# Optimization experiments

Hardware: AMD Instinct MI355X
Metric: run time of the kernel (lower is better)

Reference implementation:

```python
import jax, jax.numpy as jnp
import numpy as np

P, Q, R, H1, H2, PH, B = 32, 32, 8, 128, 64, 16, 8192
PAIRS = P * Q
OUT = PAIRS * R  # X_Z_layer output units


def _pairwise_mask(p, q, r):
    # rows i*q+k correspond to pair (x_i, z_k): connected to x_i and z_k only
    mx = np.zeros((p * q, p), np.float32)
    for i in range(p):
        mx[i * q:(i + 1) * q, i] = 1.0
    mz = np.tile(np.eye(q, dtype=np.float32), (p, 1))
    m = np.concatenate([mx, mz], axis=1)          # [p*q, p+q]
    return np.repeat(m, r, axis=0)                 # [p*q*r, p+q]


def setup_inputs() -> dict:
    key = jax.random.key(0)
    ks = jax.random.split(key, 24)
    rn = lambda k, s, sc=0.1: jax.random.normal(k, s, jnp.float32) * sc
    x = jax.random.normal(ks[0], (B, P), jnp.float32)
    z = jax.random.normal(ks[1], (B, Q), jnp.float32)
    # X_mlp: P -> H1 -> H2 -> 1
    xw1, xb1 = rn(ks[2], (P, H1)), rn(ks[3], (H1,))
    xw2, xb2 = rn(ks[4], (H1, H2)), rn(ks[5], (H2,))
    xw3, xb3 = rn(ks[6], (H2, 1)), rn(ks[7], (1,))
    # Z_mlp: Q -> H1 -> H2 -> 1
    zw1, zb1 = rn(ks[8], (Q, H1)), rn(ks[9], (H1,))
    zw2, zb2 = rn(ks[10], (Q if False else H1, H2)), rn(ks[11], (H2,))
    zw3, zb3 = rn(ks[12], (H2, 1)), rn(ks[13], (1,))
    # masked X_Z_layer: weight pre-multiplied by structured mask (as in __init__)
    mask = jnp.asarray(_pairwise_mask(P, Q, R))    # [OUT, P+Q]
    xzw = (rn(ks[14], (OUT, P + Q)) * mask).T      # [P+Q, OUT]
    xzb = rn(ks[15], (OUT,))
    # 1024 tiny per-pair MLPs: R -> PH (bias) -> 1 (no bias), stacked
    pw1 = rn(ks[16], (PAIRS, R, PH))
    pb1 = rn(ks[17], (PAIRS, PH))
    pw2 = rn(ks[18], (PAIRS, PH))
    return dict(x=x, z=z, xw1=xw1, xb1=xb1, xw2=xw2, xb2=xb2, xw3=xw3, xb3=xb3,
                zw1=zw1, zb1=zb1, zw2=zw2, zb2=zb2, zw3=zw3, zb3=zb3,
                xzw=xzw, xzb=xzb, pw1=pw1, pb1=pb1, pw2=pw2)


def reference(x, z, xw1, xb1, xw2, xb2, xw3, xb3,
              zw1, zb1, zw2, zb2, zw3, zb3, xzw, xzb, pw1, pb1, pw2):
    relu = jax.nn.relu
    # main-effect MLPs
    hx = relu(relu(x @ xw1 + xb1) @ xw2 + xb2)
    out_x = hx @ xw3 + xb3                         # [B,1]
    hz = relu(relu(z @ zw1 + zb1) @ zw2 + zb2)
    out_z = hz @ zw3 + zb3                         # [B,1]
    # masked interaction layer
    xz = jnp.concatenate([x, z], axis=1)           # [B, P+Q]
    h = relu(xz @ xzw + xzb)                       # [B, OUT]
    # all 1024 per-pair MLPs as one batched GEMM
    hp = h.reshape(h.shape[0], PAIRS, R)           # [B, pairs, R]
    t = relu(jnp.einsum('bpr,prh->bph', hp, pw1) + pb1)
    out_xz = jnp.einsum('bph,ph->b', t, pw2)[:, None]  # sum over pairs -> [B,1]
    return out_x + out_z + out_xz
```

## Files before the change

### kernel.cpp

```cpp
#include <hip/hip_runtime.h>

#define B_TOT 8192
#define PP 32
#define QQ 32
#define RR 8
#define H1 128
#define H2 64
#define PHH 16
#define PAIRS 1024
#define OUT_UNITS 8192

typedef float f32x16 __attribute__((ext_vector_type(16)));
typedef short s16x8  __attribute__((ext_vector_type(8)));

union FragU { s16x8 v; unsigned int u[4]; };

__device__ inline unsigned int pack_bf16(float lo, float hi) {
    return __builtin_amdgcn_perm(__float_as_uint(hi), __float_as_uint(lo), 0x07060302u);
}

__global__ void zero_out_k(float* __restrict__ out, int n) {
    int i = blockIdx.x * blockDim.x + threadIdx.x;
    if (i < n) out[i] = 0.f;
}

__global__ __launch_bounds__(256) void main_mlps_k(
    const float* __restrict__ x, const float* __restrict__ z,
    const float* __restrict__ xw1, const float* __restrict__ xb1,
    const float* __restrict__ xw2, const float* __restrict__ xb2,
    const float* __restrict__ xw3, const float* __restrict__ xb3,
    const float* __restrict__ zw1, const float* __restrict__ zb1,
    const float* __restrict__ zw2, const float* __restrict__ zb2,
    const float* __restrict__ zw3, const float* __restrict__ zb3,
    float* __restrict__ out)
{
    const int btile = blockIdx.x;
    const int hf    = blockIdx.y;
    const int which = blockIdx.z;
    const float* in = which ? z   : x;
    const float* w1 = which ? zw1 : xw1;
    const float* b1 = which ? zb1 : xb1;
    const float* w2 = which ? zw2 : xw2;
    const float* b2 = which ? zb2 : xb2;
    const float* w3 = which ? zw3 : xw3;
    const float* b3 = which ? zb3 : xb3;

    __shared__ float inT[32][65];
    __shared__ float h1T[128][65];

    const int t    = threadIdx.x;
    const int w    = __builtin_amdgcn_readfirstlane(t >> 6);
    const int lane = t & 63;
    const int b0   = btile * 64;

    const float4* src = reinterpret_cast<const float4*>(in + (size_t)b0 * 32);
    #pragma unroll
    for (int it = 0; it < 2; ++it) {
        int fi = t + it * 256;
        float4 v = src[fi];
        int bb = fi >> 3;
        int m  = (fi & 7) * 4;
        inT[m][bb] = v.x; inT[m+1][bb] = v.y; inT[m+2][bb] = v.z; inT[m+3][bb] = v.w;
    }
    __syncthreads();

    float h1[32];
    #pragma unroll
    for (int j = 0; j < 32; ++j) h1[j] = b1[w*32 + j];
    #pragma unroll 4
    for (int m = 0; m < 32; ++m) {
        float xv = inT[m][lane];
        #pragma unroll
        for (int j = 0; j < 32; ++j)
            h1[j] = fmaf(xv, w1[m*H1 + w*32 + j], h1[j]);
    }
    #pragma unroll
    for (int j = 0; j < 32; ++j)
        h1T[w*32 + j][lane] = fmaxf(h1[j], 0.f);
    __syncthreads();

    const int n0 = __builtin_amdgcn_readfirstlane(hf*32 + w*8);
    float h2[8];
    #pragma unroll
    for (int n = 0; n < 8; ++n) h2[n] = b2[n0 + n];
    #pragma unroll 4
    for (int m = 0; m < 128; ++m) {
        float hv = h1T[m][lane];
        #pragma unroll
        for (int n = 0; n < 8; ++n)
            h2[n] = fmaf(hv, w2[m*H2 + n0 + n], h2[n]);
    }
    float p = 0.f;
    #pragma unroll
    for (int n = 0; n < 8; ++n)
        p = fmaf(fmaxf(h2[n], 0.f), w3[n0 + n], p);
    if (hf == 0 && w == 0) p += b3[0];
    atomicAdd(out + b0 + lane, p);
}

__global__ __launch_bounds__(256, 3) void interact_k(
    const float* __restrict__ x, const float* __restrict__ z,
    const float* __restrict__ xzw, const float* __restrict__ xzb,
    const float* __restrict__ pw1, const float* __restrict__ pb1,
    const float* __restrict__ pw2, float* __restrict__ out)
{
    __shared__ float zT[16][128];
    __shared__ float4 lwx[16][2];
    __shared__ float4 lwz[16][2];
    __shared__ float4 lhb[16][2];
    __shared__ unsigned lpw1[16][4][16];
    __shared__ float lpb[16][16];
    __shared__ float lpw2[16][16];
    __shared__ float red[128][33];

    const int t     = threadIdx.x;
    const int w     = t >> 6;
    const int lane  = t & 63;
    const int m     = lane & 31;
    const int kh    = lane >> 5;
    const int jj    = m & 15;
    const int cph   = m >> 4;
    const int b0    = blockIdx.x * 128;
    const int y     = blockIdx.y;
    const int i_x   = y >> 1;
    const int k0    = (y & 1) * 16;
    const int pair0 = y * 16;

    {
        int row = t >> 1;
        int c8  = (t & 1) * 8;
        const float* src = z + (size_t)(b0 + row) * 32 + k0 + c8;
        float4 a4 = *reinterpret_cast<const float4*>(src);
        float4 b4 = *reinterpret_cast<const float4*>(src + 4);
        zT[c8+0][row] = a4.x; zT[c8+1][row] = a4.y; zT[c8+2][row] = a4.z; zT[c8+3][row] = a4.w;
        zT[c8+4][row] = b4.x; zT[c8+5][row] = b4.y; zT[c8+6][row] = b4.z; zT[c8+7][row] = b4.w;
    }
    if (t < 128) {
        int p = t >> 3, c = t & 7;
        int gp = pair0 + p;
        reinterpret_cast<float*>(lwx)[t] = xzw[(size_t)i_x * OUT_UNITS + gp*8 + c];
        reinterpret_cast<float*>(lwz)[t] = xzw[(size_t)(32 + k0 + p) * OUT_UNITS + gp*8 + c];
        reinterpret_cast<float*>(lhb)[t] = xzb[gp*8 + c];
    }
    {
        int p = t >> 4, j = t & 15;
        int gp = pair0 + p;
        lpb[p][j]  = pb1[gp*PHH + j];
        lpw2[p][j] = pw2[gp*PHH + j];
    }
    #pragma unroll
    for (int it = 0; it < 4; ++it) {
        int idx = t + it * 256;
        int p = idx >> 6, u = (idx >> 4) & 3, j = idx & 15;
        int gp = pair0 + p;
        float lo = pw1[(size_t)gp * 128 + (2*u)*16 + j];
        float hi = pw1[(size_t)gp * 128 + (2*u+1)*16 + j];
        lpw1[p][u][j] = pack_bf16(lo, hi);
    }

    const int bl  = (w & 1) * 64 + m;
    const float xv0 = x[(size_t)(b0 + bl)      * 32 + i_x];
    const float xv1 = x[(size_t)(b0 + bl + 32) * 32 + i_x];
    __syncthreads();

    f32x16 acc0, acc1, zeroC;
    #pragma unroll
    for (int r = 0; r < 16; ++r) { acc0[r] = 0.f; acc1[r] = 0.f; zeroC[r] = 0.f; }

    const bool realB = (kh == cph);
    const int  ppl0  = (w >> 1) * 4;

    #pragma unroll 2
    for (int kk = 0; kk < 4; ++kk) {
        const int ppl = ppl0 + kk;
        const int pAl = 2*ppl + kh;
        const int pBl = 2*ppl + cph;

        const float zv0 = zT[pAl][bl];
        const float zv1 = zT[pAl][bl + 32];
        const float4 wxa = lwx[pAl][0], wxb = lwx[pAl][1];
        const float4 wza = lwz[pAl][0], wzb = lwz[pAl][1];
        const float4 hba = lhb[pAl][0], hbb = lhb[pAl][1];

        float h0[8], h1[8];
        h0[0] = fmaxf(fmaf(xv0, wxa.x, fmaf(zv0, wza.x, hba.x)), 0.f);
        h0[1] = fmaxf(fmaf(xv0, wxa.y, fmaf(zv0, wza.y, hba.y)), 0.f);
        h0[2] = fmaxf(fmaf(xv0, wxa.z, fmaf(zv0, wza.z, hba.z)), 0.f);
        h0[3] = fmaxf(fmaf(xv0, wxa.w, fmaf(zv0, wza.w, hba.w)), 0.f);
        h0[4] = fmaxf(fmaf(xv0, wxb.x, fmaf(zv0, wzb.x, hbb.x)), 0.f);
        h0[5] = fmaxf(fmaf(xv0, wxb.y, fmaf(zv0, wzb.y, hbb.y)), 0.f);
        h0[6] = fmaxf(fmaf(xv0, wxb.z, fmaf(zv0, wzb.z, hbb.z)), 0.f);
        h0[7] = fmaxf(fmaf(xv0, wxb.w, fmaf(zv0, wzb.w, hbb.w)), 0.f);
        h1[0] = fmaxf(fmaf(xv1, wxa.x, fmaf(zv1, wza.x, hba.x)), 0.f);
        h1[1] = fmaxf(fmaf(xv1, wxa.y, fmaf(zv1, wza.y, hba.y)), 0.f);
        h1[2] = fmaxf(fmaf(xv1, wxa.z, fmaf(zv1, wza.z, hba.z)), 0.f);
        h1[3] = fmaxf(fmaf(xv1, wxa.w, fmaf(zv1, wza.w, hba.w)), 0.f);
        h1[4] = fmaxf(fmaf(xv1, wxb.x, fmaf(zv1, wzb.x, hbb.x)), 0.f);
        h1[5] = fmaxf(fmaf(xv1, wxb.y, fmaf(zv1, wzb.y, hbb.y)), 0.f);
        h1[6] = fmaxf(fmaf(xv1, wxb.z, fmaf(zv1, wzb.z, hbb.z)), 0.f);
        h1[7] = fmaxf(fmaf(xv1, wxb.w, fmaf(zv1, wzb.w, hbb.w)), 0.f);

        FragU a0, a1, bf;
        a0.u[0] = pack_bf16(h0[0], h0[1]);
        a0.u[1] = pack_bf16(h0[2], h0[3]);
        a0.u[2] = pack_bf16(h0[4], h0[5]);
        a0.u[3] = pack_bf16(h0[6], h0[7]);
        a1.u[0] = pack_bf16(h1[0], h1[1]);
        a1.u[1] = pack_bf16(h1[2], h1[3]);
        a1.u[2] = pack_bf16(h1[4], h1[5]);
        a1.u[3] = pack_bf16(h1[6], h1[7]);
        bf.u[0] = realB ? lpw1[pBl][0][jj] : 0u;
        bf.u[1] = realB ? lpw1[pBl][1][jj] : 0u;
        bf.u[2] = realB ? lpw1[pBl][2][jj] : 0u;
        bf.u[3] = realB ? lpw1[pBl][3][jj] : 0u;

        const float pbv = lpb[pBl][jj];
        const float w2v = lpw2[pBl][jj];

        f32x16 d0 = __builtin_amdgcn_mfma_f32_32x32x16_bf16(a0.v, bf.v, zeroC, 0, 0, 0);
        f32x16 d1 = __builtin_amdgcn_mfma_f32_32x32x16_bf16(a1.v, bf.v, zeroC, 0, 0, 0);

        #pragma unroll
        for (int r = 0; r < 16; ++r)
            acc0[r] = fmaf(fmaxf(d0[r] + pbv, 0.f), w2v, acc0[r]);
        #pragma unroll
        for (int r = 0; r < 16; ++r)
            acc1[r] = fmaf(fmaxf(d1[r] + pbv, 0.f), w2v, acc1[r]);
    }

    const int rb0 = (w & 1) * 64;
    if (w < 2) {
        #pragma unroll
        for (int r = 0; r < 16; ++r) {
            int rowf = (r & 3) + 8 * (r >> 2) + 4 * kh;
            red[rb0 + rowf][m]      = acc0[r];
            red[rb0 + 32 + rowf][m] = acc1[r];
        }
    }
    __syncthreads();
    if (w >= 2) {
        #pragma unroll
        for (int r = 0; r < 16; ++r) {
            int rowf = (r & 3) + 8 * (r >> 2) + 4 * kh;
            red[rb0 + rowf][m]      += acc0[r];
            red[rb0 + 32 + rowf][m] += acc1[r];
        }
    }
    __syncthreads();
    if (t < 128) {
        float s = 0.f;
        #pragma unroll
        for (int c = 0; c < 32; ++c) s += red[t][c];
        atomicAdd(out + b0 + t, s);
    }
}

extern "C" void kernel_launch(void* const* d_in, const int* in_sizes, int n_in,
                              void* d_out, int out_size, void* d_ws, size_t ws_size,
                              hipStream_t stream) {
    const float* x   = (const float*)d_in[0];
    const float* z   = (const float*)d_in[1];
    const float* xw1 = (const float*)d_in[2];
    const float* xb1 = (const float*)d_in[3];
    const float* xw2 = (const float*)d_in[4];
    const float* xb2 = (const float*)d_in[5];
    const float* xw3 = (const float*)d_in[6];
    const float* xb3 = (const float*)d_in[7];
    const float* zw1 = (const float*)d_in[8];
    const float* zb1 = (const float*)d_in[9];
    const float* zw2 = (const float*)d_in[10];
    const float* zb2 = (const float*)d_in[11];
    const float* zw3 = (const float*)d_in[12];
    const float* zb3 = (const float*)d_in[13];
    const float* xzw = (const float*)d_in[14];
    const float* xzb = (const float*)d_in[15];
    const float* pw1 = (const float*)d_in[16];
    const float* pb1 = (const float*)d_in[17];
    const float* pw2 = (const float*)d_in[18];
    float* out = (float*)d_out;

    zero_out_k<<<(out_size + 255) / 256, 256, 0, stream>>>(out, out_size);

    main_mlps_k<<<dim3(B_TOT / 64, 2, 2), 256, 0, stream>>>(
        x, z, xw1, xb1, xw2, xb2, xw3, xb3,
        zw1, zb1, zw2, zb2, zw3, zb3, out);

    interact_k<<<dim3(B_TOT / 128, 64), 256, 0, stream>>>(
        x, z, xzw, xzb, pw1, pb1, pw2, out);
}
```

Measured before the change: 141.0 us.

## Fuse main MLPs and interaction kernels into one launch with shared union

Merges the main-effect MLP kernel and the interaction kernel into a single launch that dispatches on block index, with shared memory overlaid through a union. The pair bias is folded into the MFMA accumulator input, main-MLP inputs are read directly into registers instead of being transposed through LDS, and the four per-wave partial sums are reduced in LDS so each block issues one atomic per row. The zeroing kernel becomes a memset. This removes a launch and the tail between the two kernels, cuts atomic traffic, and lets the small MLP blocks overlap the interaction blocks. In exchange, the occupancy hint rises from 3 to 4 blocks per CU, which may pressure registers, and the fused kernel's register use is set by the heavier branch.

```diff
diff --git a/kernel.cpp b/kernel.cpp
--- a/kernel.cpp
+++ b/kernel.cpp
@@ -10,6 +10,9 @@
 #define PAIRS 1024
 #define OUT_UNITS 8192
 
+#define NBLK_IA 4096
+#define NBLK_MM 512
+
 typedef float f32x16 __attribute__((ext_vector_type(16)));
 typedef short s16x8  __attribute__((ext_vector_type(8)));
 
@@ -19,12 +22,24 @@
     return __builtin_amdgcn_perm(__float_as_uint(hi), __float_as_uint(lo), 0x07060302u);
 }
 
-__global__ void zero_out_k(float* __restrict__ out, int n) {
-    int i = blockIdx.x * blockDim.x + threadIdx.x;
-    if (i < n) out[i] = 0.f;
-}
-
-__global__ __launch_bounds__(256) void main_mlps_k(
+union SharedU {
+    struct {
+        float zT[16][128];
+        float4 lwx[16][2];
+        float4 lwz[16][2];
+        float4 lhb[16][2];
+        unsigned lpw1[16][4][16];
+        float lpb[16][16];
+        float lpw2[16][16];
+        float red[128][33];
+    } ia;
+    struct {
+        float h1T[128][65];
+        float red2[4][64];
+    } mm;
+};
+
+__global__ __launch_bounds__(256, 4) void fused_k(
     const float* __restrict__ x, const float* __restrict__ z,
     const float* __restrict__ xw1, const float* __restrict__ xb1,
     const float* __restrict__ xw2, const float* __restrict__ xb2,
@@ -32,226 +47,224 @@
     const float* __restrict__ zw1, const float* __restrict__ zb1,
     const float* __restrict__ zw2, const float* __restrict__ zb2,
     const float* __restrict__ zw3, const float* __restrict__ zb3,
-    float* __restrict__ out)
-{
-    const int btile = blockIdx.x;
-    const int hf    = blockIdx.y;
-    const int which = blockIdx.z;
-    const float* in = which ? z   : x;
-    const float* w1 = which ? zw1 : xw1;
-    const float* b1 = which ? zb1 : xb1;
-    const float* w2 = which ? zw2 : xw2;
-    const float* b2 = which ? zb2 : xb2;
-    const float* w3 = which ? zw3 : xw3;
-    const float* b3 = which ? zb3 : xb3;
-
-    __shared__ float inT[32][65];
-    __shared__ float h1T[128][65];
-
-    const int t    = threadIdx.x;
-    const int w    = __builtin_amdgcn_readfirstlane(t >> 6);
-    const int lane = t & 63;
-    const int b0   = btile * 64;
-
-    const float4* src = reinterpret_cast<const float4*>(in + (size_t)b0 * 32);
-    #pragma unroll
-    for (int it = 0; it < 2; ++it) {
-        int fi = t + it * 256;
-        float4 v = src[fi];
-        int bb = fi >> 3;
-        int m  = (fi & 7) * 4;
-        inT[m][bb] = v.x; inT[m+1][bb] = v.y; inT[m+2][bb] = v.z; inT[m+3][bb] = v.w;
-    }
-    __syncthreads();
-
-    float h1[32];
-    #pragma unroll
-    for (int j = 0; j < 32; ++j) h1[j] = b1[w*32 + j];
-    #pragma unroll 4
-    for (int m = 0; m < 32; ++m) {
-        float xv = inT[m][lane];
-        #pragma unroll
-        for (int j = 0; j < 32; ++j)
-            h1[j] = fmaf(xv, w1[m*H1 + w*32 + j], h1[j]);
-    }
-    #pragma unroll
-    for (int j = 0; j < 32; ++j)
-        h1T[w*32 + j][lane] = fmaxf(h1[j], 0.f);
-    __syncthreads();
-
-    const int n0 = __builtin_amdgcn_readfirstlane(hf*32 + w*8);
-    float h2[8];
-    #pragma unroll
-    for (int n = 0; n < 8; ++n) h2[n] = b2[n0 + n];
-    #pragma unroll 4
-    for (int m = 0; m < 128; ++m) {
-        float hv = h1T[m][lane];
-        #pragma unroll
-        for (int n = 0; n < 8; ++n)
-            h2[n] = fmaf(hv, w2[m*H2 + n0 + n], h2[n]);
-    }
-    float p = 0.f;
-    #pragma unroll
-    for (int n = 0; n < 8; ++n)
-        p = fmaf(fmaxf(h2[n], 0.f), w3[n0 + n], p);
-    if (hf == 0 && w == 0) p += b3[0];
-    atomicAdd(out + b0 + lane, p);
-}
-
-__global__ __launch_bounds__(256, 3) void interact_k(
-    const float* __restrict__ x, const float* __restrict__ z,
     const float* __restrict__ xzw, const float* __restrict__ xzb,
     const float* __restrict__ pw1, const float* __restrict__ pb1,
     const float* __restrict__ pw2, float* __restrict__ out)
 {
-    __shared__ float zT[16][128];
-    __shared__ float4 lwx[16][2];
-    __shared__ float4 lwz[16][2];
-    __shared__ float4 lhb[16][2];
-    __shared__ unsigned lpw1[16][4][16];
-    __shared__ float lpb[16][16];
-    __shared__ float lpw2[16][16];
-    __shared__ float red[128][33];
-
-    const int t     = threadIdx.x;
-    const int w     = t >> 6;
-    const int lane  = t & 63;
-    const int m     = lane & 31;
-    const int kh    = lane >> 5;
-    const int jj    = m & 15;
-    const int cph   = m >> 4;
-    const int b0    = blockIdx.x * 128;
-    const int y     = blockIdx.y;
-    const int i_x   = y >> 1;
-    const int k0    = (y & 1) * 16;
-    const int pair0 = y * 16;
-
-    {
-        int row = t >> 1;
-        int c8  = (t & 1) * 8;
-        const float* src = z + (size_t)(b0 + row) * 32 + k0 + c8;
-        float4 a4 = *reinterpret_cast<const float4*>(src);
-        float4 b4 = *reinterpret_cast<const float4*>(src + 4);
-        zT[c8+0][row] = a4.x; zT[c8+1][row] = a4.y; zT[c8+2][row] = a4.z; zT[c8+3][row] = a4.w;
-        zT[c8+4][row] = b4.x; zT[c8+5][row] = b4.y; zT[c8+6][row] = b4.z; zT[c8+7][row] = b4.w;
-    }
-    if (t < 128) {
-        int p = t >> 3, c = t & 7;
-        int gp = pair0 + p;
-        reinterpret_cast<float*>(lwx)[t] = xzw[(size_t)i_x * OUT_UNITS + gp*8 + c];
-        reinterpret_cast<float*>(lwz)[t] = xzw[(size_t)(32 + k0 + p) * OUT_UNITS + gp*8 + c];
-        reinterpret_cast<float*>(lhb)[t] = xzb[gp*8 + c];
-    }
-    {
-        int p = t >> 4, j = t & 15;
-        int gp = pair0 + p;
-        lpb[p][j]  = pb1[gp*PHH + j];
-        lpw2[p][j] = pw2[gp*PHH + j];
-    }
-    #pragma unroll
-    for (int it = 0; it < 4; ++it) {
-        int idx = t + it * 256;
-        int p = idx >> 6, u = (idx >> 4) & 3, j = idx & 15;
-        int gp = pair0 + p;
-        float lo = pw1[(size_t)gp * 128 + (2*u)*16 + j];
-        float hi = pw1[(size_t)gp * 128 + (2*u+1)*16 + j];
-        lpw1[p][u][j] = pack_bf16(lo, hi);
-    }
-
-    const int bl  = (w & 1) * 64 + m;
-    const float xv0 = x[(size_t)(b0 + bl)      * 32 + i_x];
-    const float xv1 = x[(size_t)(b0 + bl + 32) * 32 + i_x];
-    __syncthreads();
-
-    f32x16 acc0, acc1, zeroC;
-    #pragma unroll
-    for (int r = 0; r < 16; ++r) { acc0[r] = 0.f; acc1[r] = 0.f; zeroC[r] = 0.f; }
-
-    const bool realB = (kh == cph);
-    const int  ppl0  = (w >> 1) * 4;
-
-    #pragma unroll 2
-    for (int kk = 0; kk < 4; ++kk) {
-        const int ppl = ppl0 + kk;
-        const int pAl = 2*ppl + kh;
-        const int pBl = 2*ppl + cph;
-
-        const float zv0 = zT[pAl][bl];
-        const float zv1 = zT[pAl][bl + 32];
-        const float4 wxa = lwx[pAl][0], wxb = lwx[pAl][1];
-        const float4 wza = lwz[pAl][0], wzb = lwz[pAl][1];
-        const float4 hba = lhb[pAl][0], hbb = lhb[pAl][1];
-
-        float h0[8], h1[8];
-        h0[0] = fmaxf(fmaf(xv0, wxa.x, fmaf(zv0, wza.x, hba.x)), 0.f);
-        h0[1] = fmaxf(fmaf(xv0, wxa.y, fmaf(zv0, wza.y, hba.y)), 0.f);
-        h0[2] = fmaxf(fmaf(xv0, wxa.z, fmaf(zv0, wza.z, hba.z)), 0.f);
-        h0[3] = fmaxf(fmaf(xv0, wxa.w, fmaf(zv0, wza.w, hba.w)), 0.f);
-        h0[4] = fmaxf(fmaf(xv0, wxb.x, fmaf(zv0, wzb.x, hbb.x)), 0.f);
-        h0[5] = fmaxf(fmaf(xv0, wxb.y, fmaf(zv0, wzb.y, hbb.y)), 0.f);
-        h0[6] = fmaxf(fmaf(xv0, wxb.z, fmaf(zv0, wzb.z, hbb.z)), 0.f);
-        h0[7] = fmaxf(fmaf(xv0, wxb.w, fmaf(zv0, wzb.w, hbb.w)), 0.f);
-        h1[0] = fmaxf(fmaf(xv1, wxa.x, fmaf(zv1, wza.x, hba.x)), 0.f);
-        h1[1] = fmaxf(fmaf(xv1, wxa.y, fmaf(zv1, wza.y, hba.y)), 0.f);
-        h1[2] = fmaxf(fmaf(xv1, wxa.z, fmaf(zv1, wza.z, hba.z)), 0.f);
-        h1[3] = fmaxf(fmaf(xv1, wxa.w, fmaf(zv1, wza.w, hba.w)), 0.f);
-        h1[4] = fmaxf(fmaf(xv1, wxb.x, fmaf(zv1, wzb.x, hbb.x)), 0.f);
-        h1[5] = fmaxf(fmaf(xv1, wxb.y, fmaf(zv1, wzb.y, hbb.y)), 0.f);
-        h1[6] = fmaxf(fmaf(xv1, wxb.z, fmaf(zv1, wzb.z, hbb.z)), 0.f);
-        h1[7] = fmaxf(fmaf(xv1, wxb.w, fmaf(zv1, wzb.w, hbb.w)), 0.f);
-
-        FragU a0, a1, bf;
-        a0.u[0] = pack_bf16(h0[0], h0[1]);
-        a0.u[1] = pack_bf16(h0[2], h0[3]);
-        a0.u[2] = pack_bf16(h0[4], h0[5]);
-        a0.u[3] = pack_bf16(h0[6], h0[7]);
-        a1.u[0] = pack_bf16(h1[0], h1[1]);
-        a1.u[1] = pack_bf16(h1[2], h1[3]);
-        a1.u[2] = pack_bf16(h1[4], h1[5]);
-        a1.u[3] = pack_bf16(h1[6], h1[7]);
-        bf.u[0] = realB ? lpw1[pBl][0][jj] : 0u;
-        bf.u[1] = realB ? lpw1[pBl][1][jj] : 0u;
-        bf.u[2] = realB ? lpw1[pBl][2][jj] : 0u;
-        bf.u[3] = realB ? lpw1[pBl][3][jj] : 0u;
-
-        const float pbv = lpb[pBl][jj];
-        const float w2v = lpw2[pBl][jj];
-
-        f32x16 d0 = __builtin_amdgcn_mfma_f32_32x32x16_bf16(a0.v, bf.v, zeroC, 0, 0, 0);
-        f32x16 d1 = __builtin_amdgcn_mfma_f32_32x32x16_bf16(a1.v, bf.v, zeroC, 0, 0, 0);
-
-        #pragma unroll
-        for (int r = 0; r < 16; ++r)
-            acc0[r] = fmaf(fmaxf(d0[r] + pbv, 0.f), w2v, acc0[r]);
-        #pragma unroll
-        for (int r = 0; r < 16; ++r)
-            acc1[r] = fmaf(fmaxf(d1[r] + pbv, 0.f), w2v, acc1[r]);
-    }
-
-    const int rb0 = (w & 1) * 64;
-    if (w < 2) {
-        #pragma unroll
-        for (int r = 0; r < 16; ++r) {
-            int rowf = (r & 3) + 8 * (r >> 2) + 4 * kh;
-            red[rb0 + rowf][m]      = acc0[r];
-            red[rb0 + 32 + rowf][m] = acc1[r];
-        }
-    }
-    __syncthreads();
-    if (w >= 2) {
-        #pragma unroll
-        for (int r = 0; r < 16; ++r) {
-            int rowf = (r & 3) + 8 * (r >> 2) + 4 * kh;
-            red[rb0 + rowf][m]      += acc0[r];
-            red[rb0 + 32 + rowf][m] += acc1[r];
-        }
-    }
-    __syncthreads();
-    if (t < 128) {
-        float s = 0.f;
-        #pragma unroll
-        for (int c = 0; c < 32; ++c) s += red[t][c];
-        atomicAdd(out + b0 + t, s);
+    __shared__ SharedU sh;
+    const int bid  = blockIdx.x;
+    const int t    = threadIdx.x;
+    const int w    = t >> 6;
+    const int lane = t & 63;
+
+    if (bid < NBLK_IA) {
+        const int bx    = bid & 63;
+        const int y     = bid >> 6;
+        const int m     = lane & 31;
+        const int kh    = lane >> 5;
+        const int jj    = m & 15;
+        const int cph   = m >> 4;
+        const int b0    = bx * 128;
+        const int i_x   = y >> 1;
+        const int k0    = (y & 1) * 16;
+        const int pair0 = y * 16;
+
+        {
+            int row = t >> 1;
+            int c8  = (t & 1) * 8;
+            const float* src = z + (size_t)(b0 + row) * 32 + k0 + c8;
+            float4 a4 = *reinterpret_cast<const float4*>(src);
+            float4 b4 = *reinterpret_cast<const float4*>(src + 4);
+            sh.ia.zT[c8+0][row] = a4.x; sh.ia.zT[c8+1][row] = a4.y;
+            sh.ia.zT[c8+2][row] = a4.z; sh.ia.zT[c8+3][row] = a4.w;
+            sh.ia.zT[c8+4][row] = b4.x; sh.ia.zT[c8+5][row] = b4.y;
+            sh.ia.zT[c8+6][row] = b4.z; sh.ia.zT[c8+7][row] = b4.w;
+        }
+        if (t < 128) {
+            int p = t >> 3, c = t & 7;
+            int gp = pair0 + p;
+            reinterpret_cast<float*>(sh.ia.lwx)[t] = xzw[(size_t)i_x * OUT_UNITS + gp*8 + c];
+            reinterpret_cast<float*>(sh.ia.lwz)[t] = xzw[(size_t)(32 + k0 + p) * OUT_UNITS + gp*8 + c];
+            reinterpret_cast<float*>(sh.ia.lhb)[t] = xzb[gp*8 + c];
+        }
+        {
+            int p = t >> 4, j = t & 15;
+            int gp = pair0 + p;
+            sh.ia.lpb[p][j]  = pb1[gp*PHH + j];
+            sh.ia.lpw2[p][j] = pw2[gp*PHH + j];
+        }
+        #pragma unroll
+        for (int it = 0; it < 4; ++it) {
+            int idx = t + it * 256;
+            int p = idx >> 6, u = (idx >> 4) & 3, j = idx & 15;
+            int gp = pair0 + p;
+            float lo = pw1[(size_t)gp * 128 + (2*u)*16 + j];
+            float hi = pw1[(size_t)gp * 128 + (2*u+1)*16 + j];
+            sh.ia.lpw1[p][u][j] = pack_bf16(lo, hi);
+        }
+
+        const int bl = (w & 1) * 64 + m;
+        const float xv0 = x[(size_t)(b0 + bl)      * 32 + i_x];
+        const float xv1 = x[(size_t)(b0 + bl + 32) * 32 + i_x];
+        __syncthreads();
+
+        f32x16 acc0, acc1;
+        #pragma unroll
+        for (int r = 0; r < 16; ++r) { acc0[r] = 0.f; acc1[r] = 0.f; }
+
+        const bool realB = (kh == cph);
+        const int  ppl0  = (w >> 1) * 4;
+
+        #pragma unroll 2
+        for (int kk = 0; kk < 4; ++kk) {
+            const int ppl = ppl0 + kk;
+            const int pAl = 2*ppl + kh;
+            const int pBl = 2*ppl + cph;
+
+            const float zv0 = sh.ia.zT[pAl][bl];
+            const float zv1 = sh.ia.zT[pAl][bl + 32];
+            const float4 wxa = sh.ia.lwx[pAl][0], wxb = sh.ia.lwx[pAl][1];
+            const float4 wza = sh.ia.lwz[pAl][0], wzb = sh.ia.lwz[pAl][1];
+            const float4 hba = sh.ia.lhb[pAl][0], hbb = sh.ia.lhb[pAl][1];
+
+            float h0[8], h1v[8];
+            h0[0] = fmaxf(fmaf(xv0, wxa.x, fmaf(zv0, wza.x, hba.x)), 0.f);
+            h0[1] = fmaxf(fmaf(xv0, wxa.y, fmaf(zv0, wza.y, hba.y)), 0.f);
+            h0[2] = fmaxf(fmaf(xv0, wxa.z, fmaf(zv0, wza.z, hba.z)), 0.f);
+            h0[3] = fmaxf(fmaf(xv0, wxa.w, fmaf(zv0, wza.w, hba.w)), 0.f);
+            h0[4] = fmaxf(fmaf(xv0, wxb.x, fmaf(zv0, wzb.x, hbb.x)), 0.f);
+            h0[5] = fmaxf(fmaf(xv0, wxb.y, fmaf(zv0, wzb.y, hbb.y)), 0.f);
+            h0[6] = fmaxf(fmaf(xv0, wxb.z, fmaf(zv0, wzb.z, hbb.z)), 0.f);
+            h0[7] = fmaxf(fmaf(xv0, wxb.w, fmaf(zv0, wzb.w, hbb.w)), 0.f);
+            h1v[0] = fmaxf(fmaf(xv1, wxa.x, fmaf(zv1, wza.x, hba.x)), 0.f);
+            h1v[1] = fmaxf(fmaf(xv1, wxa.y, fmaf(zv1, wza.y, hba.y)), 0.f);
+            h1v[2] = fmaxf(fmaf(xv1, wxa.z, fmaf(zv1, wza.z, hba.z)), 0.f);
+            h1v[3] = fmaxf(fmaf(xv1, wxa.w, fmaf(zv1, wza.w, hba.w)), 0.f);
+            h1v[4] = fmaxf(fmaf(xv1, wxb.x, fmaf(zv1, wzb.x, hbb.x)), 0.f);
+            h1v[5] = fmaxf(fmaf(xv1, wxb.y, fmaf(zv1, wzb.y, hbb.y)), 0.f);
+            h1v[6] = fmaxf(fmaf(xv1, wxb.z, fmaf(zv1, wzb.z, hbb.z)), 0.f);
+            h1v[7] = fmaxf(fmaf(xv1, wxb.w, fmaf(zv1, wzb.w, hbb.w)), 0.f);
+
+            FragU a0, a1, bf;
+            a0.u[0] = pack_bf16(h0[0], h0[1]);
+            a0.u[1] = pack_bf16(h0[2], h0[3]);
+            a0.u[2] = pack_bf16(h0[4], h0[5]);
+            a0.u[3] = pack_bf16(h0[6], h0[7]);
+            a1.u[0] = pack_bf16(h1v[0], h1v[1]);
+            a1.u[1] = pack_bf16(h1v[2], h1v[3]);
+            a1.u[2] = pack_bf16(h1v[4], h1v[5]);
+            a1.u[3] = pack_bf16(h1v[6], h1v[7]);
+            bf.u[0] = realB ? sh.ia.lpw1[pBl][0][jj] : 0u;
+            bf.u[1] = realB ? sh.ia.lpw1[pBl][1][jj] : 0u;
+            bf.u[2] = realB ? sh.ia.lpw1[pBl][2][jj] : 0u;
+            bf.u[3] = realB ? sh.ia.lpw1[pBl][3][jj] : 0u;
+
+            const float pbv = sh.ia.lpb[pBl][jj];
+            const float w2v = sh.ia.lpw2[pBl][jj];
+
+            f32x16 cpb;
+            #pragma unroll
+            for (int r = 0; r < 16; ++r) cpb[r] = pbv;
+
+            f32x16 d0 = __builtin_amdgcn_mfma_f32_32x32x16_bf16(a0.v, bf.v, cpb, 0, 0, 0);
+            f32x16 d1 = __builtin_amdgcn_mfma_f32_32x32x16_bf16(a1.v, bf.v, cpb, 0, 0, 0);
+
+            #pragma unroll
+            for (int r = 0; r < 16; ++r)
+                acc0[r] = fmaf(fmaxf(d0[r], 0.f), w2v, acc0[r]);
+            #pragma unroll
+            for (int r = 0; r < 16; ++r)
+                acc1[r] = fmaf(fmaxf(d1[r], 0.f), w2v, acc1[r]);
+        }
+
+        const int rb0 = (w & 1) * 64;
+        if (w < 2) {
+            #pragma unroll
+            for (int r = 0; r < 16; ++r) {
+                int rowf = (r & 3) + 8 * (r >> 2) + 4 * kh;
+                sh.ia.red[rb0 + rowf][m]      = acc0[r];
+                sh.ia.red[rb0 + 32 + rowf][m] = acc1[r];
+            }
+        }
+        __syncthreads();
+        if (w >= 2) {
+            #pragma unroll
+            for (int r = 0; r < 16; ++r) {
+                int rowf = (r & 3) + 8 * (r >> 2) + 4 * kh;
+                sh.ia.red[rb0 + rowf][m]      += acc0[r];
+                sh.ia.red[rb0 + 32 + rowf][m] += acc1[r];
+            }
+        }
+        __syncthreads();
+        if (t < 128) {
+            float s = 0.f;
+            #pragma unroll
+            for (int c = 0; c < 32; ++c) s += sh.ia.red[t][c];
+            atomicAdd(out + b0 + t, s);
+        }
+    } else {
+        const int r2    = bid - NBLK_IA;
+        const int btile = r2 & 127;
+        const int hf    = (r2 >> 7) & 1;
+        const int which = (r2 >> 8) & 1;
+        const float* in = which ? z   : x;
+        const float* w1 = which ? zw1 : xw1;
+        const float* b1 = which ? zb1 : xb1;
+        const float* w2 = which ? zw2 : xw2;
+        const float* b2 = which ? zb2 : xb2;
+        const float* w3 = which ? zw3 : xw3;
+        const float* b3 = which ? zb3 : xb3;
+
+        const int wu = __builtin_amdgcn_readfirstlane(w);
+        const int b0 = btile * 64;
+
+        float xr[32];
+        const float4* xrp = reinterpret_cast<const float4*>(in + (size_t)(b0 + lane) * 32);
+        #pragma unroll
+        for (int q = 0; q < 8; ++q) {
+            float4 v = xrp[q];
+            xr[4*q] = v.x; xr[4*q+1] = v.y; xr[4*q+2] = v.z; xr[4*q+3] = v.w;
+        }
+
+        float h1[32];
+        #pragma unroll
+        for (int j = 0; j < 32; ++j) h1[j] = b1[wu*32 + j];
+        #pragma unroll
+        for (int mm = 0; mm < 32; ++mm) {
+            float xv = xr[mm];
+            #pragma unroll
+            for (int j = 0; j < 32; ++j)
+                h1[j] = fmaf(xv, w1[mm*H1 + wu*32 + j], h1[j]);
+        }
+        #pragma unroll
+        for (int j = 0; j < 32; ++j)
+            sh.mm.h1T[wu*32 + j][lane] = fmaxf(h1[j], 0.f);
+        __syncthreads();
+
+        const int n0 = __builtin_amdgcn_readfirstlane(hf*32 + wu*8);
+        float h2[8];
+        #pragma unroll
+        for (int n = 0; n < 8; ++n) h2[n] = b2[n0 + n];
+        #pragma unroll 4
+        for (int mm = 0; mm < 128; ++mm) {
+            float hv = sh.mm.h1T[mm][lane];
+            #pragma unroll
+            for (int n = 0; n < 8; ++n)
+                h2[n] = fmaf(hv, w2[mm*H2 + n0 + n], h2[n]);
+        }
+        float p = 0.f;
+        #pragma unroll
+        for (int n = 0; n < 8; ++n)
+            p = fmaf(fmaxf(h2[n], 0.f), w3[n0 + n], p);
+
+        sh.mm.red2[wu][lane] = p;
+        __syncthreads();
+        if (wu == 0) {
+            float s = sh.mm.red2[0][lane] + sh.mm.red2[1][lane]
+                    + sh.mm.red2[2][lane] + sh.mm.red2[3][lane];
+            if (hf == 0) s += b3[0];
+            atomicAdd(out + b0 + lane, s);
+        }
     }
 }
 
@@ -279,12 +292,10 @@
     const float* pw2 = (const float*)d_in[18];
     float* out = (float*)d_out;
 
-    zero_out_k<<<(out_size + 255) / 256, 256, 0, stream>>>(out, out_size);
-
-    main_mlps_k<<<dim3(B_TOT / 64, 2, 2), 256, 0, stream>>>(
+    hipMemsetAsync(out, 0, (size_t)out_size * sizeof(float), stream);
+
+    fused_k<<<dim3(NBLK_IA + NBLK_MM), 256, 0, stream>>>(
         x, z, xw1, xb1, xw2, xb2, xw3, xb3,
-        zw1, zb1, zw2, zb2, zw3, zb3, out);
-
-    interact_k<<<dim3(B_TOT / 128, 64), 256, 0, stream>>>(
-        x, z, xzw, xzb, pw1, pb1, pw2, out);
+        zw1, zb1, zw2, zb2, zw3, zb3,
+        xzw, xzb, pw1, pb1, pw2, out);
 }
```

Measured after the change: 137.4 us. -2.6%, faster.
